# Optimization experiments

Hardware: AMD Instinct MI355X
Metric: run time of the kernel (lower is better)

Reference implementation:

```python
import jax, jax.numpy as jnp
import numpy as np


def log_g(x):
    # log of g(x) = x + 0.5 for x>=0, sigmoid(x) for x<0
    return jnp.where(x >= 0, jnp.log(jnp.maximum(x, 0) + 0.5), -jax.nn.softplus(-x))


def setup_inputs() -> dict:
    key = jax.random.key(0)
    k_x, k_w, k_o, k_b = jax.random.split(key, 4)
    B, S, D, H, O = 4, 8192, 1024, 1024, 1024
    x = jax.random.normal(k_x, (B, S, D), dtype=jnp.float32)
    # torch Linear weights: [out_features, in_features]
    w_in = jax.random.normal(k_w, (3 * H, D), dtype=jnp.float32) / np.sqrt(D)
    w_out = jax.random.normal(k_o, (O, H), dtype=jnp.float32) / np.sqrt(H)
    b_out = jax.random.normal(k_b, (O,), dtype=jnp.float32) * 0.01
    return {"x": x, "w_in": w_in, "w_out": w_out, "b_out": b_out}


def reference(x, w_in, w_out, b_out):
    B, S, D = x.shape
    H = w_in.shape[0] // 3
    z = jnp.einsum('bsd,hd->bsh', x, w_in)          # [B, S, 3H]
    f, i, h = jnp.split(z, 3, axis=-1)
    diff = jax.nn.softplus(-f) - jax.nn.softplus(-i)
    log_f = -jax.nn.softplus(diff)                  # [B, S, H]
    log_i = -jax.nn.softplus(-diff)
    log_h0 = jnp.full((B, 1, H), jnp.log(0.5), dtype=x.dtype)  # log_g(0)
    log_tilde_h = log_g(h)
    # NOTE: faithful to source -- cumsum is applied over a singleton dim
    # (identity), so a_star is just [0, log_f] along seq (no prefix sum).
    a_star = jnp.concatenate([jnp.zeros((B, 1, H), dtype=x.dtype), log_f], axis=1)  # [B, S+1, H]
    log_val = jnp.concatenate([log_h0, log_i + log_tilde_h], axis=1)                # [B, S+1, H]
    log_h = a_star + jax.lax.cumlogsumexp(log_val - a_star, axis=1)
    h_t = jnp.exp(log_h)                            # [B, S+1, H]
    out = h_t[:, -1, :] @ w_out.T + b_out           # [B, O]
    return out
```

## Files before the change

### kernel.cpp

```cpp
#include <hip/hip_runtime.h>
#include <math.h>

constexpr int B_ = 4, S_ = 8192, D_ = 1024, H_ = 1024, O_ = 1024;

typedef float f32x4  __attribute__((ext_vector_type(4)));
typedef float f32x16 __attribute__((ext_vector_type(16)));
typedef int   i32x4  __attribute__((ext_vector_type(4)));
typedef int   i32x8  __attribute__((ext_vector_type(8)));

__device__ __forceinline__ float softplusf(float x) {
    if (x > 20.f) return x;
    if (x < -20.f) return expf(x);
    return log1pf(expf(x));
}

__global__ __launch_bounds__(256) void cvt_fp8_2(
    const float* __restrict__ srcA, unsigned char* __restrict__ dstA, int nA8,
    const float* __restrict__ srcB, unsigned char* __restrict__ dstB, int nB8) {
    int i = blockIdx.x * blockDim.x + threadIdx.x;
    const float* src; unsigned char* dst; float sc;
    if (i < nA8) { src = srcA; dst = dstA; sc = 1.f; }
    else { i -= nA8; if (i >= nB8) return; src = srcB; dst = dstB; sc = 16.f; }
    const float4* s = (const float4*)src + (size_t)i * 2;
    float4 a = s[0], b = s[1];
    int lo = __builtin_amdgcn_cvt_pk_fp8_f32(a.x * sc, a.y * sc, 0, false);
    lo     = __builtin_amdgcn_cvt_pk_fp8_f32(a.z * sc, a.w * sc, lo, true);
    int hi = __builtin_amdgcn_cvt_pk_fp8_f32(b.x * sc, b.y * sc, 0, false);
    hi     = __builtin_amdgcn_cvt_pk_fp8_f32(b.z * sc, b.w * sc, hi, true);
    ((int2*)dst)[i] = make_int2(lo, hi);
}

__global__ __launch_bounds__(256) void f_exact(
    const float* __restrict__ x, const float* __restrict__ w_in,
    float* __restrict__ F_ws)
{
    const int lane = threadIdx.x & 63;
    const int pair = blockIdx.x * 4 + (threadIdx.x >> 6);
    const int b = pair >> 10, h = pair & (H_ - 1);
    const float* xr = x + ((size_t)b * S_ + (S_ - 1)) * D_;
    const float* wf = w_in + (size_t)h * D_;
    const float* wi = wf + (size_t)H_ * D_;
    float sf = 0.f, si = 0.f;
    for (int k = lane; k < D_; k += 64) {
        float xv = xr[k];
        sf = fmaf(xv, wf[k], sf);
        si = fmaf(xv, wi[k], si);
    }
    #pragma unroll
    for (int off = 32; off > 0; off >>= 1) {
        sf += __shfl_xor(sf, off, 64);
        si += __shfl_xor(si, off, 64);
    }
    if (lane == 0) {
        float af1 = 1.f + expf(-sf), ai1 = 1.f + expf(-si);
        F_ws[(size_t)b * H_ + h] = ai1 / (af1 + ai1);
    }
}

constexpr int BM = 256, BN = 64, BK = 64;
constexpr int ABYTES = BM * BK;
constexpr int BUF_BYTES = (BM + 3 * BN) * BK;
constexpr int NBUF = 4;
constexpr int SMEM_BYTES = NBUF * BUF_BYTES;

__global__ __launch_bounds__(512, 2) void gemm_fused_fp8(
    const unsigned char* __restrict__ xq, const unsigned char* __restrict__ wq,
    float* __restrict__ acc_ws)
{
    extern __shared__ unsigned char smem[];

    const int id = blockIdx.x;
    const int c8 = id & 7;
    const int q  = id >> 3;
    const int hb = q & 15;
    const int pl = q >> 4;
    const int panel = c8 * 16 + pl;
    const int sb = panel & 31;
    const int b  = panel >> 5;

    const int h0   = hb * BN;
    const int s0   = sb * BM;
    const int tid  = threadIdx.x;
    const int lane = tid & 63;
    const int wid  = tid >> 6;
    const int wm   = wid >> 1;
    const int wn   = wid & 1;
    const int l31  = lane & 31;
    const int half = lane >> 5;

    const unsigned char* gp[4];
    {
        const int rl = lane >> 2;
        const int sp = lane & 3;
        const int qq = sp ^ ((rl >> 1) & 3);
        #pragma unroll
        for (int j = 0; j < 4; ++j) {
            int u = wid * 4 + j;
            if (u < 16) {
                int row = u * 16 + rl;
                gp[j] = xq + (size_t)(b * S_ + s0 + row) * D_ + qq * 16;
            } else if (u < 28) {
                int v = u - 16;
                int row = (v & 3) * 16 + rl;
                gp[j] = wq + (size_t)(v >> 2) * (H_ * D_)
                           + (size_t)(h0 + row) * D_ + qq * 16;
            } else {
                gp[j] = xq;
            }
        }
    }
    const int wbase = wid * 4 * 1024;

    const int g2 = (l31 >> 1) & 3;
    const int sA = ((half * 2) ^ g2) * 16;
    const int aof0  = (wm * 64 + l31) * 64 + sA;
    const int aof0x = aof0 ^ 16;
    const int bof0  = ABYTES + (wn * 32 + l31) * 64 + sA;
    const int bof0x = bof0 ^ 16;

    f32x16 acc[3][2] = {};

    auto issue_dma = [&](int c) {
        if (wid < 7) {
            unsigned char* lb = smem + (c & 3) * BUF_BYTES + wbase;
            #pragma unroll
            for (int j = 0; j < 4; ++j) {
                __builtin_amdgcn_global_load_lds(
                    (const __attribute__((address_space(1))) void*)gp[j],
                    (__attribute__((address_space(3))) void*)(lb + j * 1024),
                    16, 0, 0);
                gp[j] += BK;
            }
        }
    };
    auto rd8 = [](const unsigned char* base, int o0, int o1) -> i32x8 {
        i32x4 lo = *(const i32x4*)(base + o0);
        i32x4 hi = *(const i32x4*)(base + o1);
        i32x8 r = {lo.x, lo.y, lo.z, lo.w, hi.x, hi.y, hi.z, hi.w};
        return r;
    };
    auto ld_frags = [&](int c, i32x8* af, i32x8* bf) {
        const unsigned char* bp = smem + (c & 3) * BUF_BYTES;
        af[0] = rd8(bp, aof0,        aof0x);
        af[1] = rd8(bp, aof0 + 2048, aof0x + 2048);
        bf[0] = rd8(bp, bof0,        bof0x);
        bf[1] = rd8(bp, bof0 + 4096, bof0x + 4096);
        bf[2] = rd8(bp, bof0 + 8192, bof0x + 8192);
    };
    auto do_mfma = [&](const i32x8* af, const i32x8* bf) {
        __builtin_amdgcn_s_setprio(1);
        #pragma unroll
        for (int g = 0; g < 3; ++g)
            #pragma unroll
            for (int t = 0; t < 2; ++t)
                acc[g][t] = __builtin_amdgcn_mfma_scale_f32_32x32x64_f8f6f4(
                    af[t], bf[g], acc[g][t],
                    0, 0,
                    0, 0x7F7F7F7F,
                    0, 0x7B7B7B7B);
        __builtin_amdgcn_s_setprio(0);
    };

    i32x8 afE[2], bfE[3], afO[2], bfO[3];

    issue_dma(0); issue_dma(1); issue_dma(2);
    asm volatile("s_waitcnt vmcnt(8)" ::: "memory");
    __builtin_amdgcn_sched_barrier(0);
    __builtin_amdgcn_s_barrier();
    ld_frags(0, afE, bfE);
    asm volatile("s_waitcnt vmcnt(4) lgkmcnt(0)" ::: "memory");
    __builtin_amdgcn_sched_barrier(0);
    __builtin_amdgcn_s_barrier();

    constexpr int NC = D_ / BK;
    #pragma unroll
    for (int c = 0; c < NC; ++c) {
        i32x8* afC = (c & 1) ? afO : afE;
        i32x8* bfC = (c & 1) ? bfO : bfE;
        i32x8* afN = (c & 1) ? afE : afO;
        i32x8* bfN = (c & 1) ? bfE : bfO;
        if (c + 1 < NC) ld_frags(c + 1, afN, bfN);
        if (c + 3 < NC) issue_dma(c + 3);
        do_mfma(afC, bfC);
        if (c + 1 < NC) {
            if (c + 3 < NC)
                asm volatile("s_waitcnt vmcnt(4) lgkmcnt(0)" ::: "memory");
            else if (c == NC - 3)
                asm volatile("s_waitcnt vmcnt(0) lgkmcnt(0)" ::: "memory");
            else
                asm volatile("s_waitcnt lgkmcnt(0)" ::: "memory");
            __builtin_amdgcn_sched_barrier(0);
            __builtin_amdgcn_s_barrier();
        }
    }

    __syncthreads();
    float* colsum = (float*)smem;
    if (tid < BN) colsum[tid] = 0.f;
    __syncthreads();

    float vsum = 0.f;
    #pragma unroll
    for (int t = 0; t < 2; ++t) {
        f32x16 fv = acc[0][t], iv = acc[1][t], hv = acc[2][t];
        #pragma unroll
        for (int r = 0; r < 16; ++r) {
            float ef = __expf(-fv[r]);
            float ei = __expf(-iv[r]);
            float h  = hv[r];
            float eh = __expf(h);
            float g  = (h >= 0.f) ? (h + 0.5f)
                                  : (eh * __builtin_amdgcn_rcpf(1.f + eh));
            vsum += (1.f + ef) * __builtin_amdgcn_rcpf(1.f + ei) * g;
        }
    }
    vsum += __shfl_xor(vsum, 32, 64);
    if (half == 0) atomicAdd(&colsum[wn * 32 + l31], vsum);
    __syncthreads();
    if (tid < BN)
        atomicAdd(&acc_ws[(size_t)b * H_ + h0 + tid], colsum[tid]);
}

__global__ __launch_bounds__(256) void out_gemv(
    const float* __restrict__ wout, const float* __restrict__ bout,
    const float* __restrict__ acc_ws, const float* __restrict__ F_ws,
    float* __restrict__ out)
{
    const int lane = threadIdx.x & 63;
    const int o = blockIdx.x * 4 + (threadIdx.x >> 6);
    float s[B_] = {};
    for (int h = lane; h < H_; h += 64) {
        float w = wout[(size_t)o * H_ + h];
        #pragma unroll
        for (int b = 0; b < B_; ++b) {
            float hv = F_ws[b * H_ + h] * (0.5f + acc_ws[b * H_ + h]);
            s[b] = fmaf(w, hv, s[b]);
        }
    }
    #pragma unroll
    for (int b = 0; b < B_; ++b)
        #pragma unroll
        for (int off = 32; off > 0; off >>= 1)
            s[b] += __shfl_down(s[b], off, 64);
    if (lane == 0) {
        float bo = bout[o];
        #pragma unroll
        for (int b = 0; b < B_; ++b)
            out[(size_t)b * O_ + o] = s[b] + bo;
    }
}

constexpr int TS = 64, TH = 64, TK = 16, LDP = 68;

__global__ __launch_bounds__(256) void fused_gemm_reduce(
    const float* __restrict__ x, const float* __restrict__ win,
    float* __restrict__ acc_ws, float* __restrict__ F_ws)
{
    __shared__ __align__(16) float As[TK][LDP];
    __shared__ __align__(16) float Wf[TK][LDP];
    __shared__ __align__(16) float Wi[TK][LDP];
    __shared__ __align__(16) float Wh[TK][LDP];
    __shared__ float colsum[TH];

    const int b  = blockIdx.z;
    const int s0 = blockIdx.x * TS;
    const int h0 = blockIdx.y * TH;
    const int tid = threadIdx.x;
    const int tx = tid & 15;
    const int ty = tid >> 4;

    float accf[4][4] = {};
    float acci[4][4] = {};
    float acch[4][4] = {};

    const int lrow = tid >> 2;
    const int lk4  = (tid & 3) << 2;

    const float* xp  = x   + ((size_t)b * S_ + (s0 + lrow)) * D_ + lk4;
    const float* wfp = win + (size_t)(h0 + lrow) * D_ + lk4;
    const float* wip = wfp + (size_t)H_ * D_;
    const float* whp = wip + (size_t)H_ * D_;

    for (int k0 = 0; k0 < D_; k0 += TK) {
        float4 va = *(const float4*)(xp  + k0);
        float4 vf = *(const float4*)(wfp + k0);
        float4 vi = *(const float4*)(wip + k0);
        float4 vh = *(const float4*)(whp + k0);
        __syncthreads();
        As[lk4+0][lrow]=va.x; As[lk4+1][lrow]=va.y; As[lk4+2][lrow]=va.z; As[lk4+3][lrow]=va.w;
        Wf[lk4+0][lrow]=vf.x; Wf[lk4+1][lrow]=vf.y; Wf[lk4+2][lrow]=vf.z; Wf[lk4+3][lrow]=vf.w;
        Wi[lk4+0][lrow]=vi.x; Wi[lk4+1][lrow]=vi.y; Wi[lk4+2][lrow]=vi.z; Wi[lk4+3][lrow]=vi.w;
        Wh[lk4+0][lrow]=vh.x; Wh[lk4+1][lrow]=vh.y; Wh[lk4+2][lrow]=vh.z; Wh[lk4+3][lrow]=vh.w;
        __syncthreads();
        #pragma unroll
        for (int k = 0; k < TK; ++k) {
            float4 a4 = *(const float4*)&As[k][ty << 2];
            float4 f4 = *(const float4*)&Wf[k][tx << 2];
            float4 i4 = *(const float4*)&Wi[k][tx << 2];
            float4 h4 = *(const float4*)&Wh[k][tx << 2];
            float a[4]  = {a4.x, a4.y, a4.z, a4.w};
            float wf[4] = {f4.x, f4.y, f4.z, f4.w};
            float wi[4] = {i4.x, i4.y, i4.z, i4.w};
            float wh[4] = {h4.x, h4.y, h4.z, h4.w};
            #pragma unroll
            for (int r = 0; r < 4; ++r)
                #pragma unroll
                for (int cc = 0; cc < 4; ++cc) {
                    accf[r][cc] = fmaf(a[r], wf[cc], accf[r][cc]);
                    acci[r][cc] = fmaf(a[r], wi[cc], acci[r][cc]);
                    acch[r][cc] = fmaf(a[r], wh[cc], acch[r][cc]);
                }
        }
    }

    const bool last_s = (s0 + TS == S_);
    float cval[4] = {0.f, 0.f, 0.f, 0.f};
    #pragma unroll
    for (int cc = 0; cc < 4; ++cc)
        #pragma unroll
        for (int r = 0; r < 4; ++r) {
            float f = accf[r][cc], i = acci[r][cc], h = acch[r][cc];
            float d  = softplusf(-f) - softplusf(-i);
            float lg = (h >= 0.f) ? logf(h + 0.5f) : -softplusf(-h);
            cval[cc] += expf(d + lg);
            if (last_s && ty == 15 && r == 3)
                F_ws[(size_t)b * H_ + h0 + (tx << 2) + cc] = expf(-softplusf(d));
        }
    if (tid < TH) colsum[tid] = 0.f;
    __syncthreads();
    #pragma unroll
    for (int cc = 0; cc < 4; ++cc)
        atomicAdd(&colsum[(tx << 2) + cc], cval[cc]);
    __syncthreads();
    if (tid < TH)
        atomicAdd(&acc_ws[(size_t)b * H_ + h0 + tid], colsum[tid]);
}

extern "C" void kernel_launch(void* const* d_in, const int* in_sizes, int n_in,
                              void* d_out, int out_size, void* d_ws, size_t ws_size,
                              hipStream_t stream) {
    const float* x    = (const float*)d_in[0];
    const float* w_in = (const float*)d_in[1];
    const float* wout = (const float*)d_in[2];
    const float* bout = (const float*)d_in[3];
    float* out = (float*)d_out;

    float* acc_ws = (float*)d_ws;
    float* F_ws   = acc_ws + (size_t)B_ * H_;

    hipMemsetAsync(d_ws, 0, 2 * (size_t)B_ * H_ * sizeof(float), stream);

    const size_t nx = (size_t)B_ * S_ * D_;
    const size_t nw = (size_t)3 * H_ * D_;
    const size_t q_off = 32768;
    const size_t need = q_off + nx + nw;

    if (ws_size >= need) {
        unsigned char* xq = (unsigned char*)d_ws + q_off;
        unsigned char* wq = xq + nx;
        int nx8 = (int)(nx / 8), nw8 = (int)(nw / 8);

        static int attr_done = 0;
        if (!attr_done) {
            (void)hipFuncSetAttribute((const void*)gemm_fused_fp8,
                hipFuncAttributeMaxDynamicSharedMemorySize, SMEM_BYTES);
            attr_done = 1;
        }

        cvt_fp8_2<<<(nx8 + nw8 + 255) / 256, 256, 0, stream>>>(
            x, xq, nx8, w_in, wq, nw8);
        f_exact<<<B_ * H_ / 4, 256, 0, stream>>>(x, w_in, F_ws);
        gemm_fused_fp8<<<(H_ / BN) * ((B_ * S_) / BM), 512, SMEM_BYTES, stream>>>(
            xq, wq, acc_ws);
    } else {
        dim3 grid(S_ / TS, H_ / TH, B_);
        fused_gemm_reduce<<<grid, 256, 0, stream>>>(x, w_in, acc_ws, F_ws);
    }
    out_gemv<<<O_ / 4, 256, 0, stream>>>(wout, bout, acc_ws, F_ws, out);
}
```

Before: 331.4 us.

## Interleave LDS fragment reads with MFMA groups in finer-grained software pipeline

Restructures the FP8 GEMM main loop so each K-chunk is split into three MFMA pairs, with the LDS fragment loads for the next pair issued between them and barriers placed per sub-step. DMA prefetch depth drops from three chunks ahead to two, and register usage for B fragments shrinks from double-buffered triples to three single registers. The aim is better overlap of LDS reads with matrix ops and lower register pressure. In exchange it adds more workgroup barriers and exposes more global-load latency because the prefetch distance is shorter.

```diff
diff --git a/kernel.cpp b/kernel.cpp
--- a/kernel.cpp
+++ b/kernel.cpp
@@ -139,59 +139,87 @@
         i32x8 r = {lo.x, lo.y, lo.z, lo.w, hi.x, hi.y, hi.z, hi.w};
         return r;
     };
-    auto ld_frags = [&](int c, i32x8* af, i32x8* bf) {
-        const unsigned char* bp = smem + (c & 3) * BUF_BYTES;
-        af[0] = rd8(bp, aof0,        aof0x);
-        af[1] = rd8(bp, aof0 + 2048, aof0x + 2048);
-        bf[0] = rd8(bp, bof0,        bof0x);
-        bf[1] = rd8(bp, bof0 + 4096, bof0x + 4096);
-        bf[2] = rd8(bp, bof0 + 8192, bof0x + 8192);
-    };
-    auto do_mfma = [&](const i32x8* af, const i32x8* bf) {
+
+    i32x8 afE[2], afO[2], bf0, bf1, bf2;
+
+    auto mfma2 = [&](int g, const i32x8* af, i32x8 bf) {
         __builtin_amdgcn_s_setprio(1);
-        #pragma unroll
-        for (int g = 0; g < 3; ++g)
-            #pragma unroll
-            for (int t = 0; t < 2; ++t)
-                acc[g][t] = __builtin_amdgcn_mfma_scale_f32_32x32x64_f8f6f4(
-                    af[t], bf[g], acc[g][t],
-                    0, 0,
-                    0, 0x7F7F7F7F,
-                    0, 0x7B7B7B7B);
+        acc[g][0] = __builtin_amdgcn_mfma_scale_f32_32x32x64_f8f6f4(
+            af[0], bf, acc[g][0], 0, 0, 0, 0x7F7F7F7F, 0, 0x7B7B7B7B);
+        acc[g][1] = __builtin_amdgcn_mfma_scale_f32_32x32x64_f8f6f4(
+            af[1], bf, acc[g][1], 0, 0, 0, 0x7F7F7F7F, 0, 0x7B7B7B7B);
         __builtin_amdgcn_s_setprio(0);
     };
 
-    i32x8 afE[2], bfE[3], afO[2], bfO[3];
-
-    issue_dma(0); issue_dma(1); issue_dma(2);
-    asm volatile("s_waitcnt vmcnt(8)" ::: "memory");
+    issue_dma(0);
+    issue_dma(1);
+    asm volatile("s_waitcnt vmcnt(4)" ::: "memory");
     __builtin_amdgcn_sched_barrier(0);
     __builtin_amdgcn_s_barrier();
-    ld_frags(0, afE, bfE);
-    asm volatile("s_waitcnt vmcnt(4) lgkmcnt(0)" ::: "memory");
-    __builtin_amdgcn_sched_barrier(0);
-    __builtin_amdgcn_s_barrier();
+    {
+        const unsigned char* bp = smem;
+        afE[0] = rd8(bp, aof0,        aof0x);
+        afE[1] = rd8(bp, aof0 + 2048, aof0x + 2048);
+        bf0    = rd8(bp, bof0,        bof0x);
+    }
 
     constexpr int NC = D_ / BK;
     #pragma unroll
-    for (int c = 0; c < NC; ++c) {
-        i32x8* afC = (c & 1) ? afO : afE;
-        i32x8* bfC = (c & 1) ? bfO : bfE;
-        i32x8* afN = (c & 1) ? afE : afO;
-        i32x8* bfN = (c & 1) ? bfE : bfO;
-        if (c + 1 < NC) ld_frags(c + 1, afN, bfN);
-        if (c + 3 < NC) issue_dma(c + 3);
-        do_mfma(afC, bfC);
-        if (c + 1 < NC) {
-            if (c + 3 < NC)
-                asm volatile("s_waitcnt vmcnt(4) lgkmcnt(0)" ::: "memory");
-            else if (c == NC - 3)
-                asm volatile("s_waitcnt vmcnt(0) lgkmcnt(0)" ::: "memory");
-            else
-                asm volatile("s_waitcnt lgkmcnt(0)" ::: "memory");
-            __builtin_amdgcn_sched_barrier(0);
-            __builtin_amdgcn_s_barrier();
-        }
+    for (int k = 0; k < NC / 2; ++k) {
+        const int c = 2 * k, d = 2 * k + 1;
+        const unsigned char* bc = smem + (c & 3) * BUF_BYTES;
+        const unsigned char* bd = smem + (d & 3) * BUF_BYTES;
+        const unsigned char* bn = smem + ((c + 2) & 3) * BUF_BYTES;
+        const bool more = (k < NC / 2 - 1);
+
+        bf1 = rd8(bc, bof0 + 4096, bof0x + 4096);
+        if (more) issue_dma(c + 2);
+        __builtin_amdgcn_sched_barrier(0);
+        mfma2(0, afE, bf0);
+        __builtin_amdgcn_sched_barrier(0);
+        if (more) { asm volatile("s_waitcnt vmcnt(4)" ::: "memory"); }
+        else      { asm volatile("s_waitcnt vmcnt(0)" ::: "memory"); }
+        __builtin_amdgcn_sched_barrier(0);
+        __builtin_amdgcn_s_barrier();
+
+        bf2    = rd8(bc, bof0 + 8192, bof0x + 8192);
+        afO[0] = rd8(bd, aof0,        aof0x);
+        __builtin_amdgcn_sched_barrier(0);
+        mfma2(1, afE, bf1);
+        __builtin_amdgcn_sched_barrier(0);
+        __builtin_amdgcn_s_barrier();
+
+        afO[1] = rd8(bd, aof0 + 2048, aof0x + 2048);
+        bf0    = rd8(bd, bof0,        bof0x);
+        __builtin_amdgcn_sched_barrier(0);
+        mfma2(2, afE, bf2);
+        __builtin_amdgcn_sched_barrier(0);
+        __builtin_amdgcn_s_barrier();
+
+        bf1 = rd8(bd, bof0 + 4096, bof0x + 4096);
+        if (more) issue_dma(c + 3);
+        __builtin_amdgcn_sched_barrier(0);
+        mfma2(0, afO, bf0);
+        __builtin_amdgcn_sched_barrier(0);
+        if (more) { asm volatile("s_waitcnt vmcnt(4)" ::: "memory"); }
+        __builtin_amdgcn_sched_barrier(0);
+        __builtin_amdgcn_s_barrier();
+
+        bf2 = rd8(bd, bof0 + 8192, bof0x + 8192);
+        if (more) afE[0] = rd8(bn, aof0, aof0x);
+        __builtin_amdgcn_sched_barrier(0);
+        mfma2(1, afO, bf1);
+        __builtin_amdgcn_sched_barrier(0);
+        __builtin_amdgcn_s_barrier();
+
+        if (more) {
+            afE[1] = rd8(bn, aof0 + 2048, aof0x + 2048);
+            bf0    = rd8(bn, bof0,        bof0x);
+        }
+        __builtin_amdgcn_sched_barrier(0);
+        mfma2(2, afO, bf2);
+        __builtin_amdgcn_sched_barrier(0);
+        __builtin_amdgcn_s_barrier();
     }
 
     __syncthreads();
```

After: 331.7 us. About the same (+0.1%).

## Pre-tile X in MFMA fragment layout and load A directly from global

Applied to the files above, without the earlier changes.

The fp8 conversion of x now writes into a tiled layout that matches the MFMA A-fragment order, so the GEMM kernel loads A fragments straight from global memory into registers and no longer stages them through LDS. Only the weight B tiles still go through LDS DMA, which shrinks the per-buffer LDS footprint and the number of DMA-issuing waves. The pipeline waits and barriers are reworked to match the new vmcnt accounting. The risk is that A reads from global, reused by 16 column blocks, rely on L2 hits, and the hand-tuned vmcnt counts must be exactly right.

```diff
diff --git a/kernel.cpp b/kernel.cpp
--- a/kernel.cpp
+++ b/kernel.cpp
@@ -14,19 +14,47 @@
     return log1pf(expf(x));
 }
 
-__global__ __launch_bounds__(256) void cvt_fp8_2(
-    const float* __restrict__ srcA, unsigned char* __restrict__ dstA, int nA8,
-    const float* __restrict__ srcB, unsigned char* __restrict__ dstB, int nB8) {
+__global__ __launch_bounds__(256) void cvt_x_tiled(
+    const float* __restrict__ x, unsigned char* __restrict__ xq)
+{
+    const int blk = blockIdx.x;
+    const int pp  = blk >> 2;
+    const int rq  = blk & 3;
+    const int rl  = threadIdx.x >> 2;
+    const int seg = threadIdx.x & 3;
+    const int r   = rq * 64 + rl;
+
+    const float* src = x + ((size_t)(pp * 256 + r)) * 1024 + seg * 16;
+    unsigned char* dst = xq + (size_t)pp * 262144
+                       + (r >> 5) * 2048 + (seg & 1) * 1024
+                       + (((seg >> 1) * 32 + (r & 31))) * 16;
+    #pragma unroll 4
+    for (int c = 0; c < 16; ++c) {
+        const float4* s4 = (const float4*)(src + c * 64);
+        float4 f0 = s4[0], f1 = s4[1], f2 = s4[2], f3 = s4[3];
+        int d0 = __builtin_amdgcn_cvt_pk_fp8_f32(f0.x, f0.y, 0, false);
+        d0     = __builtin_amdgcn_cvt_pk_fp8_f32(f0.z, f0.w, d0, true);
+        int d1 = __builtin_amdgcn_cvt_pk_fp8_f32(f1.x, f1.y, 0, false);
+        d1     = __builtin_amdgcn_cvt_pk_fp8_f32(f1.z, f1.w, d1, true);
+        int d2 = __builtin_amdgcn_cvt_pk_fp8_f32(f2.x, f2.y, 0, false);
+        d2     = __builtin_amdgcn_cvt_pk_fp8_f32(f2.z, f2.w, d2, true);
+        int d3 = __builtin_amdgcn_cvt_pk_fp8_f32(f3.x, f3.y, 0, false);
+        d3     = __builtin_amdgcn_cvt_pk_fp8_f32(f3.z, f3.w, d3, true);
+        *(int4*)(dst + (size_t)c * 16384) = make_int4(d0, d1, d2, d3);
+    }
+}
+
+__global__ __launch_bounds__(256) void cvt_w8(
+    const float* __restrict__ src, unsigned char* __restrict__ dst, int n8)
+{
     int i = blockIdx.x * blockDim.x + threadIdx.x;
-    const float* src; unsigned char* dst; float sc;
-    if (i < nA8) { src = srcA; dst = dstA; sc = 1.f; }
-    else { i -= nA8; if (i >= nB8) return; src = srcB; dst = dstB; sc = 16.f; }
+    if (i >= n8) return;
     const float4* s = (const float4*)src + (size_t)i * 2;
     float4 a = s[0], b = s[1];
-    int lo = __builtin_amdgcn_cvt_pk_fp8_f32(a.x * sc, a.y * sc, 0, false);
-    lo     = __builtin_amdgcn_cvt_pk_fp8_f32(a.z * sc, a.w * sc, lo, true);
-    int hi = __builtin_amdgcn_cvt_pk_fp8_f32(b.x * sc, b.y * sc, 0, false);
-    hi     = __builtin_amdgcn_cvt_pk_fp8_f32(b.z * sc, b.w * sc, hi, true);
+    int lo = __builtin_amdgcn_cvt_pk_fp8_f32(a.x * 16.f, a.y * 16.f, 0, false);
+    lo     = __builtin_amdgcn_cvt_pk_fp8_f32(a.z * 16.f, a.w * 16.f, lo, true);
+    int hi = __builtin_amdgcn_cvt_pk_fp8_f32(b.x * 16.f, b.y * 16.f, 0, false);
+    hi     = __builtin_amdgcn_cvt_pk_fp8_f32(b.z * 16.f, b.w * 16.f, hi, true);
     ((int2*)dst)[i] = make_int2(lo, hi);
 }
 
@@ -58,8 +86,7 @@
 }
 
 constexpr int BM = 256, BN = 64, BK = 64;
-constexpr int ABYTES = BM * BK;
-constexpr int BUF_BYTES = (BM + 3 * BN) * BK;
+constexpr int BUF_BYTES = 3 * BN * BK;
 constexpr int NBUF = 4;
 constexpr int SMEM_BYTES = NBUF * BUF_BYTES;
 
@@ -75,11 +102,8 @@
     const int hb = q & 15;
     const int pl = q >> 4;
     const int panel = c8 * 16 + pl;
-    const int sb = panel & 31;
-    const int b  = panel >> 5;
 
     const int h0   = hb * BN;
-    const int s0   = sb * BM;
     const int tid  = threadIdx.x;
     const int lane = tid & 63;
     const int wid  = tid >> 6;
@@ -88,50 +112,54 @@
     const int l31  = lane & 31;
     const int half = lane >> 5;
 
-    const unsigned char* gp[4];
+    const unsigned char* gpb[2];
     {
         const int rl = lane >> 2;
         const int sp = lane & 3;
         const int qq = sp ^ ((rl >> 1) & 3);
         #pragma unroll
-        for (int j = 0; j < 4; ++j) {
-            int u = wid * 4 + j;
-            if (u < 16) {
-                int row = u * 16 + rl;
-                gp[j] = xq + (size_t)(b * S_ + s0 + row) * D_ + qq * 16;
-            } else if (u < 28) {
-                int v = u - 16;
-                int row = (v & 3) * 16 + rl;
-                gp[j] = wq + (size_t)(v >> 2) * (H_ * D_)
-                           + (size_t)(h0 + row) * D_ + qq * 16;
+        for (int j = 0; j < 2; ++j) {
+            int v = wid * 2 + j;
+            if (v < 12) {
+                gpb[j] = wq + (size_t)(v >> 2) * (H_ * D_)
+                            + (size_t)(h0 + (v & 3) * 16 + rl) * D_ + qq * 16;
             } else {
-                gp[j] = xq;
+                gpb[j] = wq;
             }
         }
     }
-    const int wbase = wid * 4 * 1024;
+
+    const unsigned char* abase = xq + (size_t)panel * 262144
+                               + wm * 4096 + lane * 16;
 
     const int g2 = (l31 >> 1) & 3;
     const int sA = ((half * 2) ^ g2) * 16;
-    const int aof0  = (wm * 64 + l31) * 64 + sA;
-    const int aof0x = aof0 ^ 16;
-    const int bof0  = ABYTES + (wn * 32 + l31) * 64 + sA;
+    const int bof0  = (wn * 32 + l31) * 64 + sA;
     const int bof0x = bof0 ^ 16;
 
     f32x16 acc[3][2] = {};
 
-    auto issue_dma = [&](int c) {
-        if (wid < 7) {
-            unsigned char* lb = smem + (c & 3) * BUF_BYTES + wbase;
+    auto issueB = [&](int cc) {
+        if (wid < 6) {
+            unsigned char* lb = smem + (cc & 3) * BUF_BYTES + wid * 2048;
             #pragma unroll
-            for (int j = 0; j < 4; ++j) {
+            for (int j = 0; j < 2; ++j) {
                 __builtin_amdgcn_global_load_lds(
-                    (const __attribute__((address_space(1))) void*)gp[j],
+                    (const __attribute__((address_space(1))) void*)gpb[j],
                     (__attribute__((address_space(3))) void*)(lb + j * 1024),
                     16, 0, 0);
-                gp[j] += BK;
+                gpb[j] += BK;
             }
         }
+    };
+    auto ldA = [&](int cc, i32x8* af) {
+        const unsigned char* p = abase + (size_t)cc * 16384;
+        i32x4 a0 = *(const i32x4*)(p);
+        i32x4 a1 = *(const i32x4*)(p + 1024);
+        i32x4 a2 = *(const i32x4*)(p + 2048);
+        i32x4 a3 = *(const i32x4*)(p + 3072);
+        af[0] = (i32x8){a0.x, a0.y, a0.z, a0.w, a1.x, a1.y, a1.z, a1.w};
+        af[1] = (i32x8){a2.x, a2.y, a2.z, a2.w, a3.x, a3.y, a3.z, a3.w};
     };
     auto rd8 = [](const unsigned char* base, int o0, int o1) -> i32x8 {
         i32x4 lo = *(const i32x4*)(base + o0);
@@ -139,38 +167,22 @@
         i32x8 r = {lo.x, lo.y, lo.z, lo.w, hi.x, hi.y, hi.z, hi.w};
         return r;
     };
-    auto ld_frags = [&](int c, i32x8* af, i32x8* bf) {
-        const unsigned char* bp = smem + (c & 3) * BUF_BYTES;
-        af[0] = rd8(bp, aof0,        aof0x);
-        af[1] = rd8(bp, aof0 + 2048, aof0x + 2048);
+    auto ldB = [&](int cc, i32x8* bf) {
+        const unsigned char* bp = smem + (cc & 3) * BUF_BYTES;
         bf[0] = rd8(bp, bof0,        bof0x);
         bf[1] = rd8(bp, bof0 + 4096, bof0x + 4096);
         bf[2] = rd8(bp, bof0 + 8192, bof0x + 8192);
     };
-    auto do_mfma = [&](const i32x8* af, const i32x8* bf) {
-        __builtin_amdgcn_s_setprio(1);
-        #pragma unroll
-        for (int g = 0; g < 3; ++g)
-            #pragma unroll
-            for (int t = 0; t < 2; ++t)
-                acc[g][t] = __builtin_amdgcn_mfma_scale_f32_32x32x64_f8f6f4(
-                    af[t], bf[g], acc[g][t],
-                    0, 0,
-                    0, 0x7F7F7F7F,
-                    0, 0x7B7B7B7B);
-        __builtin_amdgcn_s_setprio(0);
-    };
-
-    i32x8 afE[2], bfE[3], afO[2], bfO[3];
-
-    issue_dma(0); issue_dma(1); issue_dma(2);
-    asm volatile("s_waitcnt vmcnt(8)" ::: "memory");
+
+    i32x8 afE[2], afO[2], bfE[3], bfO[3];
+
+    ldA(0, afE);
+    issueB(0); issueB(1); issueB(2);
+    asm volatile("s_waitcnt vmcnt(4)" ::: "memory");
     __builtin_amdgcn_sched_barrier(0);
     __builtin_amdgcn_s_barrier();
-    ld_frags(0, afE, bfE);
-    asm volatile("s_waitcnt vmcnt(4) lgkmcnt(0)" ::: "memory");
     __builtin_amdgcn_sched_barrier(0);
-    __builtin_amdgcn_s_barrier();
+    ldB(0, bfE);
 
     constexpr int NC = D_ / BK;
     #pragma unroll
@@ -179,21 +191,40 @@
         i32x8* bfC = (c & 1) ? bfO : bfE;
         i32x8* afN = (c & 1) ? afE : afO;
         i32x8* bfN = (c & 1) ? bfE : bfO;
-        if (c + 1 < NC) ld_frags(c + 1, afN, bfN);
-        if (c + 3 < NC) issue_dma(c + 3);
-        do_mfma(afC, bfC);
+
+        if (c + 1 < NC) ldA(c + 1, afN);
+        if (c + 3 < NC) issueB(c + 3);
+
         if (c + 1 < NC) {
-            if (c + 3 < NC)
-                asm volatile("s_waitcnt vmcnt(4) lgkmcnt(0)" ::: "memory");
-            else if (c == NC - 3)
-                asm volatile("s_waitcnt vmcnt(0) lgkmcnt(0)" ::: "memory");
-            else
-                asm volatile("s_waitcnt lgkmcnt(0)" ::: "memory");
+            if (wid < 6) {
+                if (c == 0)        { asm volatile("s_waitcnt vmcnt(8)"  ::: "memory"); }
+                else if (c <= 12)  { asm volatile("s_waitcnt vmcnt(12)" ::: "memory"); }
+                else if (c == 13)  { asm volatile("s_waitcnt vmcnt(10)" ::: "memory"); }
+                else               { asm volatile("s_waitcnt vmcnt(8)"  ::: "memory"); }
+            } else {
+                asm volatile("s_waitcnt vmcnt(8)" ::: "memory");
+            }
+            asm volatile("s_waitcnt lgkmcnt(0)" ::: "memory");
             __builtin_amdgcn_sched_barrier(0);
             __builtin_amdgcn_s_barrier();
-        }
-    }
-
+            __builtin_amdgcn_sched_barrier(0);
+            ldB(c + 1, bfN);
+        }
+
+        __builtin_amdgcn_s_setprio(1);
+        #pragma unroll
+        for (int g = 0; g < 3; ++g)
+            #pragma unroll
+            for (int t = 0; t < 2; ++t)
+                acc[g][t] = __builtin_amdgcn_mfma_scale_f32_32x32x64_f8f6f4(
+                    afC[t], bfC[g], acc[g][t],
+                    0, 0,
+                    0, 0x7F7F7F7F,
+                    0, 0x7B7B7B7B);
+        __builtin_amdgcn_s_setprio(0);
+    }
+
+    const int b = panel >> 5;
     __syncthreads();
     float* colsum = (float*)smem;
     if (tid < BN) colsum[tid] = 0.f;
@@ -358,7 +389,7 @@
     if (ws_size >= need) {
         unsigned char* xq = (unsigned char*)d_ws + q_off;
         unsigned char* wq = xq + nx;
-        int nx8 = (int)(nx / 8), nw8 = (int)(nw / 8);
+        int nw8 = (int)(nw / 8);
 
         static int attr_done = 0;
         if (!attr_done) {
@@ -367,8 +398,8 @@
             attr_done = 1;
         }
 
-        cvt_fp8_2<<<(nx8 + nw8 + 255) / 256, 256, 0, stream>>>(
-            x, xq, nx8, w_in, wq, nw8);
+        cvt_x_tiled<<<128 * 4, 256, 0, stream>>>(x, xq);
+        cvt_w8<<<(nw8 + 255) / 256, 256, 0, stream>>>(w_in, wq, nw8);
         f_exact<<<B_ * H_ / 4, 256, 0, stream>>>(x, w_in, F_ws);
         gemm_fused_fp8<<<(H_ / BN) * ((B_ * S_) / BM), 512, SMEM_BYTES, stream>>>(
             xq, wq, acc_ws);
```

Measured after the change: 704.9 us. 113% more time.
